# Performance work log

Hardware: AMD Instinct MI355X
Metric: run time of the kernel (lower is better)

The kernel has to match this reference:

```python
import jax, jax.numpy as jnp
import numpy as np

INPUT, HIDDEN, OUTPUT = 256, 512, 256
B, T = 64, 2048


def setup_inputs() -> dict:
    key = jax.random.key(0)
    ks = jax.random.split(key, 9)
    s_g = 1.0 / np.sqrt(INPUT + HIDDEN)  # nn.Linear default init scale
    s_o = 1.0 / np.sqrt(HIDDEN)
    u = lambda k, shape, s: jax.random.uniform(k, shape, jnp.float32, -s, s)
    return {
        "x": jax.random.normal(ks[0], (B, T, INPUT), jnp.float32),
        "hidden": jnp.zeros((1, HIDDEN), jnp.float32),
        "W_i": u(ks[1], (INPUT + HIDDEN, HIDDEN), s_g),
        "b_i": u(ks[2], (HIDDEN,), s_g),
        "W_g": u(ks[3], (INPUT + HIDDEN, HIDDEN), s_g),
        "b_g": u(ks[4], (HIDDEN,), s_g),
        "W_o": u(ks[5], (INPUT + HIDDEN, HIDDEN), s_g),
        "b_o": u(ks[6], (HIDDEN,), s_g),
        "W_out": u(ks[7], (HIDDEN, OUTPUT), s_o),
        "b_out": u(ks[8], (OUTPUT,), s_o),
    }


def reference(x, hidden, W_i, b_i, W_g, b_g, W_o, b_o, W_out, b_out):
    bs = x.shape[0]
    h0 = jnp.zeros((bs, W_i.shape[1]), x.dtype)

    def step(h, x_t):
        comb = jnp.concatenate([x_t, h], axis=-1)  # [B, input+hidden]
        i_t = jax.nn.sigmoid(comb @ W_i + b_i)
        g_t = jnp.tanh(comb @ W_g + b_g)
        o_t = jax.nn.sigmoid(comb @ W_o + b_o)
        c_t = i_t * g_t  # no forget gate: cell resets each step
        h_new = o_t * jnp.tanh(c_t)
        return h_new, None

    xT = jnp.swapaxes(x, 0, 1)  # [T, B, input]
    h_last, _ = jax.lax.scan(step, h0, xT)
    output = h_last @ W_out + b_out  # only last-step readout, as in original
    return (output, hidden)
```

## Files before the change

### kernel.cpp

```cpp
#include <hip/hip_runtime.h>
#include <hip/hip_bf16.h>

#define T_LEN 2048
#define N_IN 256
#define N_H 512
#define N_B 64

typedef float f32x4 __attribute__((ext_vector_type(4)));
typedef __bf16 bf16x8 __attribute__((ext_vector_type(8)));

__device__ __forceinline__ unsigned short f2bf(float f) {
  union { float f; unsigned int i; } x; x.f = f;
  unsigned int r = x.i + 0x7fffu + ((x.i >> 16) & 1u);
  return (unsigned short)(r >> 16);
}
__device__ __forceinline__ float sigm(float x) { return 1.0f / (1.0f + __expf(-x)); }
__device__ __forceinline__ float tanh_(float x) {
  float a = fabsf(x);
  float e = __expf(2.0f * a);
  float r = 1.0f - 2.0f / (e + 1.0f);
  return copysignf(r, x);
}
__device__ __forceinline__ bf16x8 cvt8(const float* __restrict__ p) {
  f32x4 a = *(const f32x4*)(const void*)p;
  f32x4 b = *(const f32x4*)(const void*)(p + 4);
  union { bf16x8 v; unsigned short u[8]; } r;
  #pragma unroll
  for (int j = 0; j < 4; ++j) { r.u[j] = f2bf(a[j]); r.u[j + 4] = f2bf(b[j]); }
  return r.v;
}

__global__ void lstm_init(int* __restrict__ ws) {
  int i = blockIdx.x * 256 + threadIdx.x;
  ws[i] = ((i & 16383) < 4096) ? 0 : 0x00010001;
}

__global__ __launch_bounds__(128, 1) void lstm_persist(
    const float* __restrict__ X,
    const float* __restrict__ HID,
    const float* __restrict__ Wi, const float* __restrict__ bi,
    const float* __restrict__ Wg, const float* __restrict__ bg,
    const float* __restrict__ Wo, const float* __restrict__ bo,
    const float* __restrict__ Wout, const float* __restrict__ bout,
    float* __restrict__ out,
    unsigned short* __restrict__ hbuf)
{
  extern __shared__ unsigned short ldsw[];
  unsigned short* ldsh = ldsw + 96 * 768;
  const int tid = threadIdx.x;
  const int b = blockIdx.x;
  const int g = b & 3;
  const int m = b >> 2;
  const int lane = tid & 63;
  const int wave = tid >> 6;
  const int q = lane >> 4;
  const int c = lane & 15;
  const int jb = m * 32;
  const int wcol = wave * 16;

  if (b == 0) {
    for (int i = tid; i < N_H; i += 128) out[N_B * N_IN + i] = HID[i];
  }

  for (int idx = tid; idx < 96 * 768; idx += 128) {
    int k = idx / 96, r = idx - k * 96;
    int g3 = r >> 5, cc = r & 31;
    const float* W = (g3 == 0) ? Wi : ((g3 == 1) ? Wg : Wo);
    unsigned short v = f2bf(W[k * N_H + jb + cc]);
    int byte = (r * 1536 + k * 2) ^ ((r & 7) << 4);
    *(unsigned short*)((char*)ldsw + byte) = v;
  }
  __syncthreads();

  auto ldb = [&](int gg, int kt) -> bf16x8 {
    int r = gg * 32 + wcol + c;
    int byte = (r * 1536 + kt * 64 + q * 16) ^ ((r & 7) << 4);
    return *(const bf16x8*)((const char*)ldsw + byte);
  };

  const float Bi = bi[jb + wcol + c];
  const float Bg = bg[jb + wcol + c];
  const float Bo = bo[jb + wcol + c];

  const float* xrow = X + (size_t)(g * 16 + c) * (T_LEN * N_IN);

  unsigned short* gh0 = hbuf + g * 32768;
  const int roff64 = (q >> 1) * 64 + c * 4 + (q & 1) * 2;
  const int swr = wave * 384;
  const int srb = wave * 384 + (lane >> 2) * 24 + (lane & 3) * 4;
  const unsigned long long TAGM = 0x0000000100000001ull;

  #pragma unroll 1
  for (int t = 0; t < T_LEN; ++t) {
    f32x4 ai = {0.f, 0.f, 0.f, 0.f};
    f32x4 ag = {0.f, 0.f, 0.f, 0.f};
    f32x4 ao = {0.f, 0.f, 0.f, 0.f};
    const float* xp = xrow + (size_t)t * N_IN + q * 8;
    #pragma unroll
    for (int kk = 0; kk < 8; ++kk) {
      bf16x8 a = cvt8(xp + kk * 32);
      ai = __builtin_amdgcn_mfma_f32_16x16x32_bf16(a, ldb(0, kk), ai, 0, 0, 0);
      ag = __builtin_amdgcn_mfma_f32_16x16x32_bf16(a, ldb(1, kk), ag, 0, 0, 0);
      ao = __builtin_amdgcn_mfma_f32_16x16x32_bf16(a, ldb(2, kk), ao, 0, 0, 0);
    }

    const unsigned long long* hb64 =
        (const unsigned long long*)(gh0 + (size_t)(t & 3) * 8192);
    unsigned long long hreg[32];
    {
      const unsigned long long want = ((t >> 2) & 1) ? TAGM : 0ull;
      for (;;) {
        #pragma unroll
        for (int kk = 0; kk < 16; ++kk) {
          hreg[2 * kk]     = __hip_atomic_load(hb64 + kk * 128 + roff64,
                                               __ATOMIC_RELAXED, __HIP_MEMORY_SCOPE_AGENT);
          hreg[2 * kk + 1] = __hip_atomic_load(hb64 + kk * 128 + roff64 + 1,
                                               __ATOMIC_RELAXED, __HIP_MEMORY_SCOPE_AGENT);
        }
        bool ok = true;
        #pragma unroll
        for (int i = 0; i < 32; ++i) ok &= ((hreg[i] & TAGM) == want);
        if (__all(ok)) break;
      }
    }

    #pragma unroll
    for (int kk = 0; kk < 16; ++kk) {
      union { unsigned long long u[2]; bf16x8 v; } a;
      a.u[0] = hreg[2 * kk]; a.u[1] = hreg[2 * kk + 1];
      ai = __builtin_amdgcn_mfma_f32_16x16x32_bf16(a.v, ldb(0, kk + 8), ai, 0, 0, 0);
      ag = __builtin_amdgcn_mfma_f32_16x16x32_bf16(a.v, ldb(1, kk + 8), ag, 0, 0, 0);
      ao = __builtin_amdgcn_mfma_f32_16x16x32_bf16(a.v, ldb(2, kk + 8), ao, 0, 0, 0);
    }

    const unsigned short tau1 = (unsigned short)(((t + 1) >> 2) & 1);
    #pragma unroll
    for (int j = 0; j < 4; ++j) {
      float iv = sigm(ai[j] + Bi);
      float gv = tanh_(ag[j] + Bg);
      float ov = sigm(ao[j] + Bo);
      float h = ov * tanh_(iv * gv);
      unsigned short hv = f2bf(h);
      if ((c & 1) == 0) hv = (unsigned short)((hv & 0xFFFEu) | tau1);
      ldsh[swr + (q * 4 + j) * 24 + c] = hv;
    }
    asm volatile("s_waitcnt lgkmcnt(0)" ::: "memory");
    {
      unsigned long long v64;
      __builtin_memcpy(&v64, (const void*)(ldsh + srb), 8);
      unsigned long long* hn =
          (unsigned long long*)(gh0 + (size_t)((t + 1) & 3) * 8192) + m * 128 + tid;
      __hip_atomic_store(hn, v64, __ATOMIC_RELAXED, __HIP_MEMORY_SCOPE_AGENT);
    }
  }

  if (wave == 0) {
    const unsigned long long* hb64 = (const unsigned long long*)gh0;
    unsigned long long he[32];
    for (;;) {
      #pragma unroll
      for (int kk = 0; kk < 16; ++kk) {
        he[2 * kk]     = __hip_atomic_load(hb64 + kk * 128 + roff64,
                                           __ATOMIC_RELAXED, __HIP_MEMORY_SCOPE_AGENT);
        he[2 * kk + 1] = __hip_atomic_load(hb64 + kk * 128 + roff64 + 1,
                                           __ATOMIC_RELAXED, __HIP_MEMORY_SCOPE_AGENT);
      }
      bool ok = true;
      #pragma unroll
      for (int i = 0; i < 32; ++i) ok &= ((he[i] & TAGM) == 0ull);
      if (__all(ok)) break;
    }
    f32x4 acc = {0.f, 0.f, 0.f, 0.f};
    #pragma unroll 4
    for (int kk = 0; kk < 16; ++kk) {
      union { unsigned long long u[2]; bf16x8 v; } a;
      a.u[0] = he[2 * kk]; a.u[1] = he[2 * kk + 1];
      union { bf16x8 v; unsigned short u[8]; } bb;
      #pragma unroll
      for (int j = 0; j < 8; ++j)
        bb.u[j] = f2bf(Wout[(size_t)(kk * 32 + q * 8 + j) * N_IN + m * 16 + c]);
      acc = __builtin_amdgcn_mfma_f32_16x16x32_bf16(a.v, bb.v, acc, 0, 0, 0);
    }
    const float Bb = bout[m * 16 + c];
    #pragma unroll
    for (int j = 0; j < 4; ++j) {
      int row = q * 4 + j;
      out[(g * 16 + row) * N_IN + m * 16 + c] = acc[j] + Bb;
    }
  }
}

extern "C" void kernel_launch(void* const* d_in, const int* in_sizes, int n_in,
                              void* d_out, int out_size, void* d_ws, size_t ws_size,
                              hipStream_t stream) {
  const float* X    = (const float*)d_in[0];
  const float* HID  = (const float*)d_in[1];
  const float* Wi   = (const float*)d_in[2];
  const float* bi   = (const float*)d_in[3];
  const float* Wg   = (const float*)d_in[4];
  const float* bg   = (const float*)d_in[5];
  const float* Wo   = (const float*)d_in[6];
  const float* bo   = (const float*)d_in[7];
  const float* Wout = (const float*)d_in[8];
  const float* bout = (const float*)d_in[9];

  unsigned short* hbuf = (unsigned short*)d_ws;

  lstm_init<<<dim3(256), dim3(256), 0, stream>>>((int*)d_ws);
  lstm_persist<<<dim3(64), dim3(128), 96 * 768 * 2 + 1536, stream>>>(
      X, HID, Wi, bi, Wg, bg, Wo, bo, Wout, bout,
      (float*)d_out, hbuf);
}
```

Measured before the change: 6.942 ms.

## Co-locate each batch group's blocks on one XCD and use XCD-local sc0 h exchange

```diff
diff --git a/kernel.cpp b/kernel.cpp
--- a/kernel.cpp
+++ b/kernel.cpp
@@ -8,6 +8,7 @@
 
 typedef float f32x4 __attribute__((ext_vector_type(4)));
 typedef __bf16 bf16x8 __attribute__((ext_vector_type(8)));
+typedef int i32x4 __attribute__((ext_vector_type(4)));
 
 __device__ __forceinline__ unsigned short f2bf(float f) {
   union { float f; unsigned int i; } x; x.f = f;
@@ -30,27 +31,83 @@
   return r.v;
 }
 
-__global__ void lstm_init(int* __restrict__ ws) {
+__device__ __forceinline__ void st_u64_sc0(void* sb, int vb, unsigned long long v) {
+  asm volatile("global_store_dwordx2 %0, %1, %2 sc0"
+               :: "v"(vb), "v"(v), "s"(sb) : "memory");
+}
+__device__ __forceinline__ void ld_h16_sc0(const void* sb, int vb, i32x4 f[16]) {
+  int v0 = vb, v1 = vb + 4096, v2 = vb + 8192, v3 = vb + 12288;
+  asm volatile(
+    "global_load_dwordx4 %0, %16, %20 offset:0 sc0\n\t"
+    "global_load_dwordx4 %1, %16, %20 offset:1024 sc0\n\t"
+    "global_load_dwordx4 %2, %16, %20 offset:2048 sc0\n\t"
+    "global_load_dwordx4 %3, %16, %20 offset:3072 sc0\n\t"
+    "global_load_dwordx4 %4, %17, %20 offset:0 sc0\n\t"
+    "global_load_dwordx4 %5, %17, %20 offset:1024 sc0\n\t"
+    "global_load_dwordx4 %6, %17, %20 offset:2048 sc0\n\t"
+    "global_load_dwordx4 %7, %17, %20 offset:3072 sc0\n\t"
+    "global_load_dwordx4 %8, %18, %20 offset:0 sc0\n\t"
+    "global_load_dwordx4 %9, %18, %20 offset:1024 sc0\n\t"
+    "global_load_dwordx4 %10, %18, %20 offset:2048 sc0\n\t"
+    "global_load_dwordx4 %11, %18, %20 offset:3072 sc0\n\t"
+    "global_load_dwordx4 %12, %19, %20 offset:0 sc0\n\t"
+    "global_load_dwordx4 %13, %19, %20 offset:1024 sc0\n\t"
+    "global_load_dwordx4 %14, %19, %20 offset:2048 sc0\n\t"
+    "global_load_dwordx4 %15, %19, %20 offset:3072 sc0\n\t"
+    "s_waitcnt vmcnt(0)"
+    : "=&v"(f[0]), "=&v"(f[1]), "=&v"(f[2]), "=&v"(f[3]),
+      "=&v"(f[4]), "=&v"(f[5]), "=&v"(f[6]), "=&v"(f[7]),
+      "=&v"(f[8]), "=&v"(f[9]), "=&v"(f[10]), "=&v"(f[11]),
+      "=&v"(f[12]), "=&v"(f[13]), "=&v"(f[14]), "=&v"(f[15])
+    : "v"(v0), "v"(v1), "v"(v2), "v"(v3), "s"(sb)
+    : "memory");
+}
+
+__global__ void lstm_init(int* __restrict__ ws, int nInts) {
   int i = blockIdx.x * 256 + threadIdx.x;
-  ws[i] = ((i & 16383) < 4096) ? 0 : 0x00010001;
+  if (i >= nInts) return;
+  if (i < 1024) { ws[i] = (i >= 64 && i < 192) ? -1 : 0; return; }
+  int j = i - 1024;
+  ws[i] = ((j & 16383) < 4096) ? 0 : 0x00010001;
 }
 
 __global__ __launch_bounds__(128, 1) void lstm_persist(
-    const float* __restrict__ X,
-    const float* __restrict__ HID,
+    const float* __restrict__ X, const float* __restrict__ HID,
     const float* __restrict__ Wi, const float* __restrict__ bi,
     const float* __restrict__ Wg, const float* __restrict__ bg,
     const float* __restrict__ Wo, const float* __restrict__ bo,
     const float* __restrict__ Wout, const float* __restrict__ bout,
     float* __restrict__ out,
-    unsigned short* __restrict__ hbuf)
+    unsigned short* __restrict__ hbF, unsigned short* __restrict__ hbS,
+    int* __restrict__ reg, int dual)
 {
   extern __shared__ unsigned short ldsw[];
   unsigned short* ldsh = ldsw + 96 * 768;
+  __shared__ int sh_gid, sh_m;
   const int tid = threadIdx.x;
-  const int b = blockIdx.x;
-  const int g = b & 3;
-  const int m = b >> 2;
+
+  if (tid == 0) {
+    unsigned xcc;
+    asm volatile("s_getreg_b32 %0, hwreg(HW_REG_XCC_ID)" : "=s"(xcc));
+    xcc &= 7;
+    int s = __hip_atomic_fetch_add(&reg[8 + xcc], 1, __ATOMIC_RELAXED, __HIP_MEMORY_SCOPE_AGENT);
+    int batch = s >> 4;
+    if ((s & 15) == 15) {
+      int gid = __hip_atomic_fetch_add(&reg[1], 1, __ATOMIC_RELAXED, __HIP_MEMORY_SCOPE_AGENT);
+      __hip_atomic_store(&reg[64 + (int)xcc * 16 + batch], (gid < 4) ? gid : 99,
+                         __ATOMIC_RELAXED, __HIP_MEMORY_SCOPE_AGENT);
+    }
+    __hip_atomic_fetch_add(&reg[0], 1, __ATOMIC_RELEASE, __HIP_MEMORY_SCOPE_AGENT);
+    while (__hip_atomic_load(&reg[0], __ATOMIC_ACQUIRE, __HIP_MEMORY_SCOPE_AGENT) < 256) {}
+    sh_gid = __hip_atomic_load(&reg[64 + (int)xcc * 16 + batch],
+                               __ATOMIC_RELAXED, __HIP_MEMORY_SCOPE_AGENT);
+    sh_m = s & 15;
+  }
+  __syncthreads();
+  const int gid = sh_gid;
+  const int m = sh_m;
+  if (gid < 0 || gid >= 4) return;
+
   const int lane = tid & 63;
   const int wave = tid >> 6;
   const int q = lane >> 4;
@@ -58,7 +115,7 @@
   const int jb = m * 32;
   const int wcol = wave * 16;
 
-  if (b == 0) {
+  if (gid == 0 && m == 0) {
     for (int i = tid; i < N_H; i += 128) out[N_B * N_IN + i] = HID[i];
   }
 
@@ -81,14 +138,16 @@
   const float Bi = bi[jb + wcol + c];
   const float Bg = bg[jb + wcol + c];
   const float Bo = bo[jb + wcol + c];
-
-  const float* xrow = X + (size_t)(g * 16 + c) * (T_LEN * N_IN);
-
-  unsigned short* gh0 = hbuf + g * 32768;
+  const float* xrow = X + (size_t)(gid * 16 + c) * (T_LEN * N_IN);
+
+  char* const gf = (char*)hbF + gid * 65536;
+  char* const gs = (char*)hbS + gid * 65536;
   const int roff64 = (q >> 1) * 64 + c * 4 + (q & 1) * 2;
+  const int vbr = (q >> 1) * 512 + c * 32 + (q & 1) * 16;
   const int swr = wave * 384;
   const int srb = wave * 384 + (lane >> 2) * 24 + (lane & 3) * 4;
   const unsigned long long TAGM = 0x0000000100000001ull;
+  bool slow = !dual;
 
   #pragma unroll 1
   for (int t = 0; t < T_LEN; ++t) {
@@ -104,11 +163,27 @@
       ao = __builtin_amdgcn_mfma_f32_16x16x32_bf16(a, ldb(2, kk), ao, 0, 0, 0);
     }
 
-    const unsigned long long* hb64 =
-        (const unsigned long long*)(gh0 + (size_t)(t & 3) * 8192);
     unsigned long long hreg[32];
-    {
-      const unsigned long long want = ((t >> 2) & 1) ? TAGM : 0ull;
+    const unsigned long long want = ((t >> 2) & 1) ? TAGM : 0ull;
+    bool got = false;
+    if (!slow) {
+      const char* fb = gf + (t & 3) * 16384;
+      for (int tries = 0; tries < 4096 && !got; ++tries) {
+        i32x4 f[16];
+        ld_h16_sc0(fb, vbr, f);
+        bool ok = true;
+        #pragma unroll
+        for (int kk = 0; kk < 16; ++kk) {
+          union { i32x4 i; unsigned long long u[2]; } w; w.i = f[kk];
+          hreg[2 * kk] = w.u[0]; hreg[2 * kk + 1] = w.u[1];
+          ok &= ((w.u[0] & TAGM) == want) & ((w.u[1] & TAGM) == want);
+        }
+        if (__all(ok)) got = true;
+      }
+      if (!got) slow = true;
+    }
+    if (!got) {
+      const unsigned long long* hb64 = (const unsigned long long*)(void*)(gs + (t & 3) * 16384);
       for (;;) {
         #pragma unroll
         for (int kk = 0; kk < 16; ++kk) {
@@ -148,27 +223,45 @@
     {
       unsigned long long v64;
       __builtin_memcpy(&v64, (const void*)(ldsh + srb), 8);
-      unsigned long long* hn =
-          (unsigned long long*)(gh0 + (size_t)((t + 1) & 3) * 8192) + m * 128 + tid;
-      __hip_atomic_store(hn, v64, __ATOMIC_RELAXED, __HIP_MEMORY_SCOPE_AGENT);
+      st_u64_sc0(gf + ((t + 1) & 3) * 16384, m * 1024 + tid * 8, v64);
+      unsigned long long* ds =
+          (unsigned long long*)(void*)(gs + ((t + 1) & 3) * 16384) + m * 128 + tid;
+      __hip_atomic_store(ds, v64, __ATOMIC_RELAXED, __HIP_MEMORY_SCOPE_AGENT);
     }
   }
 
   if (wave == 0) {
-    const unsigned long long* hb64 = (const unsigned long long*)gh0;
     unsigned long long he[32];
-    for (;;) {
-      #pragma unroll
-      for (int kk = 0; kk < 16; ++kk) {
-        he[2 * kk]     = __hip_atomic_load(hb64 + kk * 128 + roff64,
-                                           __ATOMIC_RELAXED, __HIP_MEMORY_SCOPE_AGENT);
-        he[2 * kk + 1] = __hip_atomic_load(hb64 + kk * 128 + roff64 + 1,
-                                           __ATOMIC_RELAXED, __HIP_MEMORY_SCOPE_AGENT);
+    bool got = false;
+    if (!slow) {
+      for (int tries = 0; tries < 4096 && !got; ++tries) {
+        i32x4 f[16];
+        ld_h16_sc0(gf, vbr, f);
+        bool ok = true;
+        #pragma unroll
+        for (int kk = 0; kk < 16; ++kk) {
+          union { i32x4 i; unsigned long long u[2]; } w; w.i = f[kk];
+          he[2 * kk] = w.u[0]; he[2 * kk + 1] = w.u[1];
+          ok &= ((w.u[0] & TAGM) == 0ull) & ((w.u[1] & TAGM) == 0ull);
+        }
+        if (__all(ok)) got = true;
       }
-      bool ok = true;
-      #pragma unroll
-      for (int i = 0; i < 32; ++i) ok &= ((he[i] & TAGM) == 0ull);
-      if (__all(ok)) break;
+    }
+    if (!got) {
+      const unsigned long long* hb64 = (const unsigned long long*)(void*)gs;
+      for (;;) {
+        #pragma unroll
+        for (int kk = 0; kk < 16; ++kk) {
+          he[2 * kk]     = __hip_atomic_load(hb64 + kk * 128 + roff64,
+                                             __ATOMIC_RELAXED, __HIP_MEMORY_SCOPE_AGENT);
+          he[2 * kk + 1] = __hip_atomic_load(hb64 + kk * 128 + roff64 + 1,
+                                             __ATOMIC_RELAXED, __HIP_MEMORY_SCOPE_AGENT);
+        }
+        bool ok = true;
+        #pragma unroll
+        for (int i = 0; i < 32; ++i) ok &= ((he[i] & TAGM) == 0ull);
+        if (__all(ok)) break;
+      }
     }
     f32x4 acc = {0.f, 0.f, 0.f, 0.f};
     #pragma unroll 4
@@ -185,7 +278,7 @@
     #pragma unroll
     for (int j = 0; j < 4; ++j) {
       int row = q * 4 + j;
-      out[(g * 16 + row) * N_IN + m * 16 + c] = acc[j] + Bb;
+      out[(gid * 16 + row) * N_IN + m * 16 + c] = acc[j] + Bb;
     }
   }
 }
@@ -204,10 +297,15 @@
   const float* Wout = (const float*)d_in[8];
   const float* bout = (const float*)d_in[9];
 
-  unsigned short* hbuf = (unsigned short*)d_ws;
-
-  lstm_init<<<dim3(256), dim3(256), 0, stream>>>((int*)d_ws);
-  lstm_persist<<<dim3(64), dim3(128), 96 * 768 * 2 + 1536, stream>>>(
+  const size_t SET = 262144;
+  int dual = (ws_size >= 4096 + 2 * SET) ? 1 : 0;
+  int* regp = (int*)d_ws;
+  unsigned short* hbF = (unsigned short*)((char*)d_ws + 4096);
+  unsigned short* hbS = dual ? (unsigned short*)((char*)d_ws + 4096 + SET) : hbF;
+
+  int nInts = (int)((4096 + (dual ? 2 : 1) * SET) / 4);
+  lstm_init<<<dim3((nInts + 255) / 256), dim3(256), 0, stream>>>((int*)d_ws, nInts);
+  lstm_persist<<<dim3(256), dim3(128), 96 * 768 * 2 + 1536, stream>>>(
       X, HID, Wi, bi, Wg, bg, Wo, bo, Wout, bout,
-      (float*)d_out, hbuf);
-}
+      (float*)d_out, hbF, hbS, regp, dual);
+}
```

After: 17.22 ms. 2.48x slower.

## Hold gate weights in registers and halve block count to 32 four-wave blocks

Applied to the files above, without the earlier changes.

```diff
diff --git a/kernel.cpp b/kernel.cpp
--- a/kernel.cpp
+++ b/kernel.cpp
@@ -35,7 +35,7 @@
   ws[i] = ((i & 16383) < 4096) ? 0 : 0x00010001;
 }
 
-__global__ __launch_bounds__(128, 1) void lstm_persist(
+__global__ __launch_bounds__(256, 1) void lstm_persist(
     const float* __restrict__ X,
     const float* __restrict__ HID,
     const float* __restrict__ Wi, const float* __restrict__ bi,
@@ -45,8 +45,7 @@
     float* __restrict__ out,
     unsigned short* __restrict__ hbuf)
 {
-  extern __shared__ unsigned short ldsw[];
-  unsigned short* ldsh = ldsw + 96 * 768;
+  __shared__ unsigned short ldsh[4 * 384];
   const int tid = threadIdx.x;
   const int b = blockIdx.x;
   const int g = b & 3;
@@ -55,32 +54,29 @@
   const int wave = tid >> 6;
   const int q = lane >> 4;
   const int c = lane & 15;
-  const int jb = m * 32;
-  const int wcol = wave * 16;
+  const int colW = m * 64 + wave * 16 + c;
 
   if (b == 0) {
-    for (int i = tid; i < N_H; i += 128) out[N_B * N_IN + i] = HID[i];
-  }
-
-  for (int idx = tid; idx < 96 * 768; idx += 128) {
-    int k = idx / 96, r = idx - k * 96;
-    int g3 = r >> 5, cc = r & 31;
-    const float* W = (g3 == 0) ? Wi : ((g3 == 1) ? Wg : Wo);
-    unsigned short v = f2bf(W[k * N_H + jb + cc]);
-    int byte = (r * 1536 + k * 2) ^ ((r & 7) << 4);
-    *(unsigned short*)((char*)ldsw + byte) = v;
-  }
-  __syncthreads();
-
-  auto ldb = [&](int gg, int kt) -> bf16x8 {
-    int r = gg * 32 + wcol + c;
-    int byte = (r * 1536 + kt * 64 + q * 16) ^ ((r & 7) << 4);
-    return *(const bf16x8*)((const char*)ldsw + byte);
-  };
-
-  const float Bi = bi[jb + wcol + c];
-  const float Bg = bg[jb + wcol + c];
-  const float Bo = bo[jb + wcol + c];
+    for (int i = tid; i < N_H; i += 256) out[N_B * N_IN + i] = HID[i];
+  }
+
+  bf16x8 w[3][24];
+  #pragma unroll
+  for (int gg = 0; gg < 3; ++gg) {
+    const float* W = (gg == 0) ? Wi : ((gg == 1) ? Wg : Wo);
+    #pragma unroll
+    for (int kt = 0; kt < 24; ++kt) {
+      union { bf16x8 v; unsigned short u[8]; } t;
+      #pragma unroll
+      for (int j = 0; j < 8; ++j)
+        t.u[j] = f2bf(W[(size_t)(kt * 32 + q * 8 + j) * N_H + colW]);
+      w[gg][kt] = t.v;
+    }
+  }
+
+  const float Bi = bi[colW];
+  const float Bg = bg[colW];
+  const float Bo = bo[colW];
 
   const float* xrow = X + (size_t)(g * 16 + c) * (T_LEN * N_IN);
 
@@ -99,9 +95,9 @@
     #pragma unroll
     for (int kk = 0; kk < 8; ++kk) {
       bf16x8 a = cvt8(xp + kk * 32);
-      ai = __builtin_amdgcn_mfma_f32_16x16x32_bf16(a, ldb(0, kk), ai, 0, 0, 0);
-      ag = __builtin_amdgcn_mfma_f32_16x16x32_bf16(a, ldb(1, kk), ag, 0, 0, 0);
-      ao = __builtin_amdgcn_mfma_f32_16x16x32_bf16(a, ldb(2, kk), ao, 0, 0, 0);
+      ai = __builtin_amdgcn_mfma_f32_16x16x32_bf16(a, w[0][kk], ai, 0, 0, 0);
+      ag = __builtin_amdgcn_mfma_f32_16x16x32_bf16(a, w[1][kk], ag, 0, 0, 0);
+      ao = __builtin_amdgcn_mfma_f32_16x16x32_bf16(a, w[2][kk], ao, 0, 0, 0);
     }
 
     const unsigned long long* hb64 =
@@ -128,9 +124,9 @@
     for (int kk = 0; kk < 16; ++kk) {
       union { unsigned long long u[2]; bf16x8 v; } a;
       a.u[0] = hreg[2 * kk]; a.u[1] = hreg[2 * kk + 1];
-      ai = __builtin_amdgcn_mfma_f32_16x16x32_bf16(a.v, ldb(0, kk + 8), ai, 0, 0, 0);
-      ag = __builtin_amdgcn_mfma_f32_16x16x32_bf16(a.v, ldb(1, kk + 8), ag, 0, 0, 0);
-      ao = __builtin_amdgcn_mfma_f32_16x16x32_bf16(a.v, ldb(2, kk + 8), ao, 0, 0, 0);
+      ai = __builtin_amdgcn_mfma_f32_16x16x32_bf16(a.v, w[0][kk + 8], ai, 0, 0, 0);
+      ag = __builtin_amdgcn_mfma_f32_16x16x32_bf16(a.v, w[1][kk + 8], ag, 0, 0, 0);
+      ao = __builtin_amdgcn_mfma_f32_16x16x32_bf16(a.v, w[2][kk + 8], ao, 0, 0, 0);
     }
 
     const unsigned short tau1 = (unsigned short)(((t + 1) >> 2) & 1);
@@ -149,12 +145,12 @@
       unsigned long long v64;
       __builtin_memcpy(&v64, (const void*)(ldsh + srb), 8);
       unsigned long long* hn =
-          (unsigned long long*)(gh0 + (size_t)((t + 1) & 3) * 8192) + m * 128 + tid;
+          (unsigned long long*)(gh0 + (size_t)((t + 1) & 3) * 8192) + m * 256 + tid;
       __hip_atomic_store(hn, v64, __ATOMIC_RELAXED, __HIP_MEMORY_SCOPE_AGENT);
     }
   }
 
-  if (wave == 0) {
+  if (m < 4) {
     const unsigned long long* hb64 = (const unsigned long long*)gh0;
     unsigned long long he[32];
     for (;;) {
@@ -170,6 +166,7 @@
       for (int i = 0; i < 32; ++i) ok &= ((he[i] & TAGM) == 0ull);
       if (__all(ok)) break;
     }
+    const int oc = m * 64 + wave * 16 + c;
     f32x4 acc = {0.f, 0.f, 0.f, 0.f};
     #pragma unroll 4
     for (int kk = 0; kk < 16; ++kk) {
@@ -178,14 +175,14 @@
       union { bf16x8 v; unsigned short u[8]; } bb;
       #pragma unroll
       for (int j = 0; j < 8; ++j)
-        bb.u[j] = f2bf(Wout[(size_t)(kk * 32 + q * 8 + j) * N_IN + m * 16 + c]);
+        bb.u[j] = f2bf(Wout[(size_t)(kk * 32 + q * 8 + j) * N_IN + oc]);
       acc = __builtin_amdgcn_mfma_f32_16x16x32_bf16(a.v, bb.v, acc, 0, 0, 0);
     }
-    const float Bb = bout[m * 16 + c];
+    const float Bb = bout[oc];
     #pragma unroll
     for (int j = 0; j < 4; ++j) {
       int row = q * 4 + j;
-      out[(g * 16 + row) * N_IN + m * 16 + c] = acc[j] + Bb;
+      out[(g * 16 + row) * N_IN + oc] = acc[j] + Bb;
     }
   }
 }
@@ -207,7 +204,7 @@
   unsigned short* hbuf = (unsigned short*)d_ws;
 
   lstm_init<<<dim3(256), dim3(256), 0, stream>>>((int*)d_ws);
-  lstm_persist<<<dim3(64), dim3(128), 96 * 768 * 2 + 1536, stream>>>(
+  lstm_persist<<<dim3(32), dim3(256), 0, stream>>>(
       X, HID, Wi, bi, Wg, bg, Wo, bo, Wout, bout,
       (float*)d_out, hbuf);
 }
```

New measurement: 10.01 ms. +44.2%, slower.
